# Performance work log

Measured on AMD Instinct MI355X. Metric: run time of the kernel, lower is better.

Reference implementation:

```python
import jax, jax.numpy as jnp
from jax import lax
import numpy as np

B, T, NCLS, D = 64, 2048, 20, 2048
LCS_LEN, FSD_LEN = 64, 32
LAMB1, LAMB2, LAMB3 = 1.0, 5e-5, 8e-5
LAMB_LCS, LAMB_FSD = 0.01, 0.01
FEAT_MARGIN = 50.0
THRES = 0.5
GAMMA = 0.1


def cos_sim(a, b):
    a = a / jnp.linalg.norm(a, axis=1, keepdims=True)
    b = b / jnp.linalg.norm(b, axis=1, keepdims=True)
    return a @ b.T


def dp_fsd(c0, c1):
    # soft-LCS/DTW-style recurrence with maxGamma (soft max) over 3 neighbors
    h = c0.shape[-1] // 2
    m = cos_sim(c0[:, :h], c1[:, :h])  # [L, L]
    g = cos_sim(c0[:, h:], c1[:, h:])  # [L, L]
    L = m.shape[0]

    def row_step(prev_row, mg):
        m_row, g_row = mg
        diag = prev_row[:-1]  # C[i-1, j-1]
        up = prev_row[1:]     # C[i-1, j]

        def col_step(left, xs):  # left = C[i, j-1]
            d, u, mij, gij = xs
            neigh = jnp.stack([d, gij + u, gij + left])
            val = mij + GAMMA * jax.nn.logsumexp(neigh / GAMMA)
            return val, val

        _, row_vals = lax.scan(col_step, jnp.zeros((), m.dtype), (diag, up, m_row, g_row))
        new_row = jnp.concatenate([jnp.zeros((1,), m.dtype), row_vals])
        return new_row, None

    final_row, _ = lax.scan(row_step, jnp.zeros(L + 1, m.dtype), (m, g))
    return final_row[-1]


def dp_lcs(c0, c1):
    s = cos_sim(c0, c1)  # [L, L]
    L = s.shape[0]

    def row_step(prev_row, s_row):
        diag = prev_row[:-1]
        up = prev_row[1:]

        def col_step(left, xs):
            d, u, sij = xs
            val = jnp.where(sij > THRES, d + sij, jnp.maximum(u, left))
            return val, val

        _, row_vals = lax.scan(col_step, jnp.zeros((), s.dtype), (diag, up, s_row))
        return jnp.concatenate([jnp.zeros((1,), s.dtype), row_vals]), None

    final_row, _ = lax.scan(row_step, jnp.zeros(L + 1, s.dtype), s)
    return final_row[-1]


def cls_criterion(p, lab):
    return -jnp.mean(jnp.sum(jnp.log(p + 1e-10) * lab, axis=1))


def forward_once(ai_cls, ac_cls, ab_cls, vlab, att, ai_feat, ac_feat, ab_feat, ai_cas):
    bs = ai_cls.shape[0]
    ones = jnp.ones((bs, 1), ai_cls.dtype)
    zeros = jnp.zeros((bs, 1), ai_cls.dtype)
    inst_lab = jnp.concatenate([vlab, zeros], axis=1)
    cont_lab = jnp.concatenate([vlab, ones], axis=1)
    back_lab = jnp.concatenate([jnp.zeros_like(vlab), ones], axis=1)
    inst_lab = inst_lab / jnp.sum(inst_lab, axis=1, keepdims=True)
    cont_lab = cont_lab / jnp.sum(cont_lab, axis=1, keepdims=True)
    back_lab = back_lab / jnp.sum(back_lab, axis=1, keepdims=True)

    inst_loss = cls_criterion(ai_cls, inst_lab)
    cont_loss = cls_criterion(ac_cls, cont_lab)
    back_loss = cls_criterion(ab_cls, back_lab)

    guide_loss = jnp.mean(jnp.sum(jnp.abs(1.0 - ai_cas[:, :, -1] - lax.stop_gradient(att[:, :, 0])), axis=1))

    n_inst = jnp.linalg.norm(ai_feat, axis=1)
    n_cont = jnp.linalg.norm(ac_feat, axis=1)
    n_back = jnp.linalg.norm(ab_feat, axis=1)
    f1 = jnp.maximum(FEAT_MARGIN - n_inst + n_cont, 0.0)
    f2 = jnp.maximum(FEAT_MARGIN - n_cont + n_back, 0.0)
    f3 = n_back
    feat_loss = jnp.mean((f1 + f2 + f3) ** 2)

    sparse_loss = jnp.mean(jnp.sum(att[:, :, :2], axis=1))

    cls_loss = inst_loss + cont_loss + back_loss  # THUMOS14 weights 1/1/1
    return cls_loss + LAMB1 * guide_loss + LAMB2 * feat_loss + LAMB3 * sparse_loss


def _pair_loss(vals, pair_label):
    bs = vals.shape[0]
    pos = jnp.sum(vals * pair_label)
    neg = jnp.sum(vals * (1.0 - pair_label))
    pos_num = jnp.sum(pair_label)
    neg_num = bs - pos_num
    return neg / (neg_num + 1e-10) - pos / (pos_num + 1e-10)


def ftcl_forward(act_inst_cls_0, act_cont_cls_0, act_back_cls_0, vid_label_0, temp_att_0,
                 act_inst_feat_0, act_cont_feat_0, act_back_feat_0, act_inst_cas_0,
                 lcs_candi_0, fsd_act_candi_0, fsd_bak_candi_0,
                 act_inst_cls_1, act_cont_cls_1, act_back_cls_1, vid_label_1, temp_att_1,
                 act_inst_feat_1, act_cont_feat_1, act_back_feat_1, act_inst_cas_1,
                 lcs_candi_1, fsd_act_candi_1, fsd_bak_candi_1):
    loss_0 = forward_once(act_inst_cls_0, act_cont_cls_0, act_back_cls_0, vid_label_0, temp_att_0,
                          act_inst_feat_0, act_cont_feat_0, act_back_feat_0, act_inst_cas_0)
    loss_1 = forward_once(act_inst_cls_1, act_cont_cls_1, act_back_cls_1, vid_label_1, temp_att_1,
                          act_inst_feat_1, act_cont_feat_1, act_back_feat_1, act_inst_cas_1)
    acm_loss = (loss_0 + loss_1) / 2.0

    pair_label = (jnp.sum(vid_label_0 * vid_label_1, axis=1) > 0).astype(jnp.float32)  # [B]

    lcs = jax.vmap(dp_lcs)(lcs_candi_0, lcs_candi_1)  # [B]
    lcs_loss = _pair_loss(lcs, pair_label)

    # pair==1 -> act_1, pair==0 -> bak_1 (matches the per-sample branch in torch)
    fsd_c1 = jnp.where(pair_label[:, None, None] > 0, fsd_act_candi_1, fsd_bak_candi_1)
    fsd = jax.vmap(dp_fsd)(fsd_act_candi_0, fsd_c1)  # [B]
    fsd_loss = _pair_loss(fsd, pair_label)

    return acm_loss + LAMB_LCS * lcs_loss + LAMB_FSD * fsd_loss


def setup_inputs() -> dict:
    key = jax.random.key(0)
    ks = iter(jax.random.split(key, 32))
    rand = lambda s: jax.random.uniform(next(ks), s, jnp.float32)
    randn = lambda s: jax.random.normal(next(ks), s, jnp.float32)
    inp = {}
    for sfx in ('0', '1'):
        inp[f'act_inst_cls_{sfx}'] = rand((B, NCLS + 1))
        inp[f'act_cont_cls_{sfx}'] = rand((B, NCLS + 1))
        inp[f'act_back_cls_{sfx}'] = rand((B, NCLS + 1))
        inp[f'vid_label_{sfx}'] = jnp.ones((B, NCLS), jnp.float32)
        inp[f'temp_att_{sfx}'] = rand((B, T, 3))
        inp[f'act_inst_feat_{sfx}'] = randn((B, D))
        inp[f'act_cont_feat_{sfx}'] = randn((B, D))
        inp[f'act_back_feat_{sfx}'] = randn((B, D))
        inp[f'act_inst_cas_{sfx}'] = rand((B, T, NCLS + 1))
        inp[f'lcs_candi_{sfx}'] = randn((B, LCS_LEN, D))
        inp[f'fsd_act_candi_{sfx}'] = randn((B, FSD_LEN, D))
        inp[f'fsd_bak_candi_{sfx}'] = randn((B, FSD_LEN, D))
    return inp


def reference(act_inst_cls_0, act_cont_cls_0, act_back_cls_0, vid_label_0, temp_att_0,
              act_inst_feat_0, act_cont_feat_0, act_back_feat_0, act_inst_cas_0,
              lcs_candi_0, fsd_act_candi_0, fsd_bak_candi_0,
              act_inst_cls_1, act_cont_cls_1, act_back_cls_1, vid_label_1, temp_att_1,
              act_inst_feat_1, act_cont_feat_1, act_back_feat_1, act_inst_cas_1,
              lcs_candi_1, fsd_act_candi_1, fsd_bak_candi_1):
    return ftcl_forward(act_inst_cls_0, act_cont_cls_0, act_back_cls_0, vid_label_0, temp_att_0,
                        act_inst_feat_0, act_cont_feat_0, act_back_feat_0, act_inst_cas_0,
                        lcs_candi_0, fsd_act_candi_0, fsd_bak_candi_0,
                        act_inst_cls_1, act_cont_cls_1, act_back_cls_1, vid_label_1, temp_att_1,
                        act_inst_feat_1, act_cont_feat_1, act_back_feat_1, act_inst_cas_1,
                        lcs_candi_1, fsd_act_candi_1, fsd_bak_candi_1)
```

## Files before the change

### kernel.cpp

```cpp
#include <hip/hip_runtime.h>
#include <math.h>

#define Bn 64
#define Tn 2048
#define NCLS 20
#define Dn 2048
#define LCSL 64
#define FSDL 32

#define KS_L 8
#define KS_F 4

#define WS_ACC 0
#define WS_PAIR 4
#define WS_LCS 68
#define WS_FSD 132
#define WS_NORM 196
#define WS_LSQ 580
#define WS_FSQ 66116
#define WS_SPART 98884
#define WS_MG 2196036

__global__ __launch_bounds__(256) void fused_small_kernel(
    const float* __restrict__ cas0, const float* __restrict__ att0,
    const float* __restrict__ cas1, const float* __restrict__ att1,
    const float* __restrict__ f0, const float* __restrict__ f1,
    const float* __restrict__ f2, const float* __restrict__ f3,
    const float* __restrict__ f4, const float* __restrict__ f5,
    const float* __restrict__ vid0, const float* __restrict__ vid1,
    float* __restrict__ ws) {
    const int gb = blockIdx.x;
    const int t = threadIdx.x;
    if (gb < 512) {
        const int N = Bn * Tn;
        float g0 = 0.f, s0 = 0.f, g1 = 0.f, s1 = 0.f;
        for (int n = gb * 256 + t; n < 2 * N; n += 512 * 256) {
            int sfx = (n >= N);
            int m = sfx ? (n - N) : n;
            const float* cas = sfx ? cas1 : cas0;
            const float* att = sfx ? att1 : att0;
            float a0 = att[m * 3 + 0];
            float a1 = att[m * 3 + 1];
            float g = fabsf(1.0f - cas[m * (NCLS + 1) + NCLS] - a0);
            float s = a0 + a1;
            if (sfx) { g1 += g; s1 += s; } else { g0 += g; s0 += s; }
        }
        __shared__ float red[256];
        float vals[4] = {g0, s0, g1, s1};
        for (int v = 0; v < 4; ++v) {
            red[t] = vals[v];
            __syncthreads();
            for (int o = 128; o; o >>= 1) {
                if (t < o) red[t] += red[t + o];
                __syncthreads();
            }
            if (t == 0) atomicAdd(&ws[WS_ACC + v], red[0]);
            __syncthreads();
        }
    } else if (gb < 608) {
        int R = (gb - 512) * 4 + (t >> 6);
        int lane = t & 63;
        const float* arr[6] = {f0, f1, f2, f3, f4, f5};
        const float* p = arr[R >> 6] + (size_t)(R & 63) * Dn;
        float s = 0.f;
        #pragma unroll
        for (int q = 0; q < 8; ++q) {
            float4 v = *(const float4*)(p + q * 256 + lane * 4);
            s += v.x * v.x + v.y * v.y + v.z * v.z + v.w * v.w;
        }
        for (int off = 32; off; off >>= 1) s += __shfl_down(s, off);
        if (lane == 0) ws[WS_NORM + R] = sqrtf(s);
    } else {
        if (t < Bn) {
            float s = 0.f;
            for (int c = 0; c < NCLS; ++c) s += vid0[t * NCLS + c] * vid1[t * NCLS + c];
            ws[WS_PAIR + t] = (s > 0.f) ? 1.f : 0.f;
        }
    }
}

__global__ __launch_bounds__(256) void gemm_kernel(const float* __restrict__ cand0,
                                                   const float* __restrict__ cand1,
                                                   const float* __restrict__ act0,
                                                   const float* __restrict__ act1,
                                                   const float* __restrict__ bak1,
                                                   float* __restrict__ ws) {
    __shared__ float tA[64 * 66];
    __shared__ float tB[64 * 66];
    const int t = threadIdx.x;

    if (blockIdx.x < 512) {
        const int b = blockIdx.x >> 3;
        const int ks = blockIdx.x & 7;
        const float* c0 = cand0 + (size_t)b * LCSL * Dn + ks * 256;
        const float* c1 = cand1 + (size_t)b * LCSL * Dn + ks * 256;

        const int ti = t >> 4, tj = t & 15;
        const int i0 = ti * 4, j0 = tj * 4;
        float acc[4][4] = {};
        float sqa[4] = {}, sqb[4] = {};

        for (int kc = 0; kc < 256; kc += 64) {
            #pragma unroll
            for (int l = 0; l < 4; ++l) {
                int idx4 = l * 256 + t;
                int row = idx4 >> 4;
                int kq = (idx4 & 15) * 4;
                float4 av = *(const float4*)(c0 + (size_t)row * Dn + kc + kq);
                float4 bv = *(const float4*)(c1 + (size_t)row * Dn + kc + kq);
                tA[(kq + 0) * 66 + row] = av.x;
                tA[(kq + 1) * 66 + row] = av.y;
                tA[(kq + 2) * 66 + row] = av.z;
                tA[(kq + 3) * 66 + row] = av.w;
                tB[(kq + 0) * 66 + row] = bv.x;
                tB[(kq + 1) * 66 + row] = bv.y;
                tB[(kq + 2) * 66 + row] = bv.z;
                tB[(kq + 3) * 66 + row] = bv.w;
                sqa[l] += av.x * av.x + av.y * av.y + av.z * av.z + av.w * av.w;
                sqb[l] += bv.x * bv.x + bv.y * bv.y + bv.z * bv.z + bv.w * bv.w;
            }
            __syncthreads();
            #pragma unroll 8
            for (int k = 0; k < 64; ++k) {
                float2 a0v = *(const float2*)&tA[k * 66 + i0];
                float2 a1v = *(const float2*)&tA[k * 66 + i0 + 2];
                float2 b0v = *(const float2*)&tB[k * 66 + j0];
                float2 b1v = *(const float2*)&tB[k * 66 + j0 + 2];
                float a[4] = {a0v.x, a0v.y, a1v.x, a1v.y};
                float bb[4] = {b0v.x, b0v.y, b1v.x, b1v.y};
                #pragma unroll
                for (int r = 0; r < 4; ++r)
                    #pragma unroll
                    for (int c = 0; c < 4; ++c)
                        acc[r][c] = fmaf(a[r], bb[c], acc[r][c]);
            }
            __syncthreads();
        }
        float* dst = ws + WS_SPART + (size_t)(ks * Bn + b) * 4096;
        #pragma unroll
        for (int r = 0; r < 4; ++r) {
            float4 v = {acc[r][0], acc[r][1], acc[r][2], acc[r][3]};
            *(float4*)(dst + (i0 + r) * 64 + j0) = v;
        }
        #pragma unroll
        for (int l = 0; l < 4; ++l) {
            float sa = sqa[l], sb = sqb[l];
            for (int m = 1; m < 16; m <<= 1) {
                sa += __shfl_xor(sa, m);
                sb += __shfl_xor(sb, m);
            }
            if ((t & 15) == 0) {
                int row = l * 16 + (t >> 4);
                ws[WS_LSQ + ks * 8192 + b * 128 + row] = sa;
                ws[WS_LSQ + ks * 8192 + b * 128 + 64 + row] = sb;
            }
        }
    } else {
        const int q = blockIdx.x - 512;
        const int b = q >> 3;
        const int half = (q >> 2) & 1;
        const int ks = q & 3;
        const float* pairp = ws + WS_PAIR;
        const int sel = (pairp[b] > 0.f) ? 1 : 2;
        const float* c0 = act0 + (size_t)b * FSDL * Dn + half * 1024 + ks * 256;
        const float* c1 = ((sel == 1) ? act1 : bak1) + (size_t)b * FSDL * Dn + half * 1024 + ks * 256;

        const int ti = t >> 4, tj = t & 15;
        const int i0 = ti * 2, j0 = tj * 2;
        float acc[2][2] = {};
        float sqa[2] = {}, sqb[2] = {};

        for (int kc = 0; kc < 256; kc += 64) {
            #pragma unroll
            for (int l = 0; l < 2; ++l) {
                int idx4 = l * 256 + t;
                int row = idx4 >> 4;
                int kq = (idx4 & 15) * 4;
                float4 av = *(const float4*)(c0 + (size_t)row * Dn + kc + kq);
                float4 bv = *(const float4*)(c1 + (size_t)row * Dn + kc + kq);
                tA[(kq + 0) * 34 + row] = av.x;
                tA[(kq + 1) * 34 + row] = av.y;
                tA[(kq + 2) * 34 + row] = av.z;
                tA[(kq + 3) * 34 + row] = av.w;
                tB[(kq + 0) * 34 + row] = bv.x;
                tB[(kq + 1) * 34 + row] = bv.y;
                tB[(kq + 2) * 34 + row] = bv.z;
                tB[(kq + 3) * 34 + row] = bv.w;
                sqa[l] += av.x * av.x + av.y * av.y + av.z * av.z + av.w * av.w;
                sqb[l] += bv.x * bv.x + bv.y * bv.y + bv.z * bv.z + bv.w * bv.w;
            }
            __syncthreads();
            #pragma unroll 8
            for (int k = 0; k < 64; ++k) {
                float2 a = *(const float2*)&tA[k * 34 + i0];
                float2 bb = *(const float2*)&tB[k * 34 + j0];
                acc[0][0] = fmaf(a.x, bb.x, acc[0][0]);
                acc[0][1] = fmaf(a.x, bb.y, acc[0][1]);
                acc[1][0] = fmaf(a.y, bb.x, acc[1][0]);
                acc[1][1] = fmaf(a.y, bb.y, acc[1][1]);
            }
            __syncthreads();
        }
        float* dst = ws + WS_MG + (size_t)ks * 131072 + b * 2048 + half * 1024;
        #pragma unroll
        for (int r = 0; r < 2; ++r) {
            float2 v = {acc[r][0], acc[r][1]};
            *(float2*)(dst + (i0 + r) * 32 + j0) = v;
        }
        #pragma unroll
        for (int l = 0; l < 2; ++l) {
            float sa = sqa[l], sb = sqb[l];
            for (int m = 1; m < 16; m <<= 1) {
                sa += __shfl_xor(sa, m);
                sb += __shfl_xor(sb, m);
            }
            if ((t & 15) == 0) {
                int row = l * 16 + (t >> 4);
                ws[WS_FSQ + ks * 8192 + b * 128 + half * 64 + row] = sa;
                ws[WS_FSQ + ks * 8192 + b * 128 + half * 64 + 32 + row] = sb;
            }
        }
    }
}

__global__ __launch_bounds__(64) void dp_kernel(float* __restrict__ ws) {
    const int t = threadIdx.x;
    if (blockIdx.x < 64) {
        const int b = blockIdx.x;
        __shared__ float S[64 * 66];
        __shared__ float i0s[64], i1s[64];
        {
            float s0 = 0.f, s1 = 0.f;
            #pragma unroll
            for (int ks = 0; ks < KS_L; ++ks) {
                s0 += ws[WS_LSQ + ks * 8192 + b * 128 + t];
                s1 += ws[WS_LSQ + ks * 8192 + b * 128 + 64 + t];
            }
            i0s[t] = 1.0f / sqrtf(s0);
            i1s[t] = 1.0f / sqrtf(s1);
        }
        __syncthreads();
        const float* sp = ws + WS_SPART + b * 4096;
        for (int qd = 0; qd < 16; ++qd) {
            int idx4 = t + 64 * qd;
            int i = idx4 >> 4;
            int j = (idx4 & 15) * 4;
            float4 v = {0.f, 0.f, 0.f, 0.f};
            #pragma unroll
            for (int ks = 0; ks < KS_L; ++ks) {
                float4 p = *(const float4*)(sp + (size_t)ks * 262144 + idx4 * 4);
                v.x += p.x; v.y += p.y; v.z += p.z; v.w += p.w;
            }
            float ri = i0s[i];
            S[i * 66 + j + 0] = v.x * ri * i1s[j + 0];
            S[i * 66 + j + 1] = v.y * ri * i1s[j + 1];
            S[i * 66 + j + 2] = v.z * ri * i1s[j + 2];
            S[i * 66 + j + 3] = v.w * ri * i1s[j + 3];
        }
        __syncthreads();
        float prev = 0.f, prevprev = 0.f;
        float sval_next = S[t * 66 + 0];
        for (int d = 2; d <= 128; ++d) {
            float s = sval_next;
            int jn = d - t - 1;
            if (jn >= 0 && jn < 64) sval_next = S[t * 66 + jn];
            float up = __shfl_up(prev, 1);
            float dg = __shfl_up(prevprev, 1);
            if (t == 0) { up = 0.f; dg = 0.f; }
            int j = d - t - 1;
            float left = prev;
            float val = (s > 0.5f) ? (dg + s) : fmaxf(up, left);
            float cur = (j >= 1 && j <= 64) ? val : 0.f;
            prevprev = prev;
            prev = cur;
        }
        if (t == 63) ws[WS_LCS + b] = prev;
    } else {
        const int b = blockIdx.x - 64;
        __shared__ float M[32 * 34], G[32 * 34];
        __shared__ float inv[128];
        {
            #pragma unroll
            for (int e2 = 0; e2 < 2; ++e2) {
                int e = t + e2 * 64;
                float s = 0.f;
                #pragma unroll
                for (int ks = 0; ks < KS_F; ++ks)
                    s += ws[WS_FSQ + ks * 8192 + b * 128 + e];
                inv[e] = 1.0f / sqrtf(s);
            }
        }
        __syncthreads();
        const float* mg = ws + WS_MG + b * 2048;
        for (int qd = 0; qd < 4; ++qd) {
            int idx4 = t + 64 * qd;
            int i = idx4 >> 3;
            int j = (idx4 & 7) * 4;
            float4 vM = {0.f, 0.f, 0.f, 0.f}, vG = {0.f, 0.f, 0.f, 0.f};
            #pragma unroll
            for (int ks = 0; ks < KS_F; ++ks) {
                float4 pM = *(const float4*)(mg + (size_t)ks * 131072 + idx4 * 4);
                float4 pG = *(const float4*)(mg + (size_t)ks * 131072 + 1024 + idx4 * 4);
                vM.x += pM.x; vM.y += pM.y; vM.z += pM.z; vM.w += pM.w;
                vG.x += pG.x; vG.y += pG.y; vG.z += pG.z; vG.w += pG.w;
            }
            float riM = inv[i], riG = inv[64 + i];
            M[i * 34 + j + 0] = vM.x * riM * inv[32 + j + 0];
            M[i * 34 + j + 1] = vM.y * riM * inv[32 + j + 1];
            M[i * 34 + j + 2] = vM.z * riM * inv[32 + j + 2];
            M[i * 34 + j + 3] = vM.w * riM * inv[32 + j + 3];
            G[i * 34 + j + 0] = vG.x * riG * inv[96 + j + 0];
            G[i * 34 + j + 1] = vG.y * riG * inv[96 + j + 1];
            G[i * 34 + j + 2] = vG.z * riG * inv[96 + j + 2];
            G[i * 34 + j + 3] = vG.w * riG * inv[96 + j + 3];
        }
        __syncthreads();
        if (t < 32) {
            float prev = 0.f, prevprev = 0.f;
            float m_next = M[t * 34 + 0], g_next = G[t * 34 + 0];
            for (int d = 2; d <= 64; ++d) {
                float m = m_next, g = g_next;
                int jn = d - t - 1;
                if (jn >= 0 && jn < 32) { m_next = M[t * 34 + jn]; g_next = G[t * 34 + jn]; }
                float up = __shfl_up(prev, 1);
                float dg = __shfl_up(prevprev, 1);
                if (t == 0) { up = 0.f; dg = 0.f; }
                int j = d - t - 1;
                float left = prev;
                float x0 = dg * 10.0f;
                float x1 = (g + up) * 10.0f;
                float x2 = (g + left) * 10.0f;
                float mx = fmaxf(x0, fmaxf(x1, x2));
                float lse = mx + __logf(__expf(x0 - mx) + __expf(x1 - mx) + __expf(x2 - mx));
                float val = m + 0.1f * lse;
                float cur = (j >= 1 && j <= 32) ? val : 0.f;
                prevprev = prev;
                prev = cur;
            }
            if (t == 31) ws[WS_FSD + b] = prev;
        }
    }
}

__device__ float block_reduce(float v, float* red, int t) {
    red[t] = v;
    __syncthreads();
    for (int o = 128; o; o >>= 1) {
        if (t < o) red[t] += red[t + o];
        __syncthreads();
    }
    float r = red[0];
    __syncthreads();
    return r;
}

__global__ __launch_bounds__(256) void final_kernel(
    const float* __restrict__ ai0, const float* __restrict__ ac0,
    const float* __restrict__ ab0, const float* __restrict__ vid0,
    const float* __restrict__ ai1, const float* __restrict__ ac1,
    const float* __restrict__ ab1, const float* __restrict__ vid1,
    const float* __restrict__ ws, float* __restrict__ out) {
    __shared__ float rs0[Bn], rs1[Bn];
    __shared__ float red[256];
    int t = threadIdx.x;
    if (t < Bn) {
        float s0 = 0.f, s1 = 0.f;
        for (int c = 0; c < NCLS; ++c) { s0 += vid0[t * NCLS + c]; s1 += vid1[t * NCLS + c]; }
        rs0[t] = s0;
        rs1[t] = s1;
    }
    __syncthreads();

    float inst0 = 0.f, cont0 = 0.f, back0 = 0.f;
    float inst1 = 0.f, cont1 = 0.f, back1 = 0.f;
    for (int idx = t; idx < Bn * (NCLS + 1); idx += 256) {
        int b = idx / (NCLS + 1), c = idx % (NCLS + 1);
        float v0 = (c < NCLS) ? vid0[b * NCLS + c] : 0.f;
        float v1 = (c < NCLS) ? vid1[b * NCLS + c] : 0.f;
        float wI0 = (c < NCLS) ? (v0 / rs0[b]) : 0.f;
        float wC0 = ((c < NCLS) ? v0 : 1.f) / (rs0[b] + 1.f);
        float wI1 = (c < NCLS) ? (v1 / rs1[b]) : 0.f;
        float wC1 = ((c < NCLS) ? v1 : 1.f) / (rs1[b] + 1.f);
        inst0 += logf(ai0[idx] + 1e-10f) * wI0;
        cont0 += logf(ac0[idx] + 1e-10f) * wC0;
        inst1 += logf(ai1[idx] + 1e-10f) * wI1;
        cont1 += logf(ac1[idx] + 1e-10f) * wC1;
        if (c == NCLS) {
            back0 += logf(ab0[idx] + 1e-10f);
            back1 += logf(ab1[idx] + 1e-10f);
        }
    }
    float sInst0 = block_reduce(inst0, red, t);
    float sCont0 = block_reduce(cont0, red, t);
    float sBack0 = block_reduce(back0, red, t);
    float sInst1 = block_reduce(inst1, red, t);
    float sCont1 = block_reduce(cont1, red, t);
    float sBack1 = block_reduce(back1, red, t);

    float fv0 = 0.f, fv1 = 0.f;
    if (t < Bn) {
        const float* nm = ws + WS_NORM;
        {
            float ni = nm[0 * Bn + t], nc = nm[1 * Bn + t], nb = nm[2 * Bn + t];
            float f1 = fmaxf(50.0f - ni + nc, 0.f);
            float f2 = fmaxf(50.0f - nc + nb, 0.f);
            float f = f1 + f2 + nb;
            fv0 = f * f;
        }
        {
            float ni = nm[3 * Bn + t], nc = nm[4 * Bn + t], nb = nm[5 * Bn + t];
            float f1 = fmaxf(50.0f - ni + nc, 0.f);
            float f2 = fmaxf(50.0f - nc + nb, 0.f);
            float f = f1 + f2 + nb;
            fv1 = f * f;
        }
    }
    float sFeat0 = block_reduce(fv0, red, t) / (float)Bn;
    float sFeat1 = block_reduce(fv1, red, t) / (float)Bn;

    float posL = 0.f, negL = 0.f, posF = 0.f, negF = 0.f, pln = 0.f;
    if (t < Bn) {
        float pl = ws[WS_PAIR + t];
        float lv = ws[WS_LCS + t];
        float fv = ws[WS_FSD + t];
        posL = lv * pl; negL = lv * (1.f - pl);
        posF = fv * pl; negF = fv * (1.f - pl);
        pln = pl;
    }
    float sPosL = block_reduce(posL, red, t);
    float sNegL = block_reduce(negL, red, t);
    float sPosF = block_reduce(posF, red, t);
    float sNegF = block_reduce(negF, red, t);
    float sPln = block_reduce(pln, red, t);

    if (t == 0) {
        float cls0 = -(sInst0 + sCont0 + sBack0) / (float)Bn;
        float cls1 = -(sInst1 + sCont1 + sBack1) / (float)Bn;
        float guide0 = ws[WS_ACC + 0] / (float)Bn;
        float sparse0 = ws[WS_ACC + 1] / (float)(Bn * 2);
        float guide1 = ws[WS_ACC + 2] / (float)Bn;
        float sparse1 = ws[WS_ACC + 3] / (float)(Bn * 2);
        float loss0 = cls0 + 1.0f * guide0 + 5e-05f * sFeat0 + 8e-05f * sparse0;
        float loss1 = cls1 + 1.0f * guide1 + 5e-05f * sFeat1 + 8e-05f * sparse1;
        float acm = 0.5f * (loss0 + loss1);
        float posn = sPln;
        float negn = (float)Bn - posn;
        float lcs_loss = sNegL / (negn + 1e-10f) - sPosL / (posn + 1e-10f);
        float fsd_loss = sNegF / (negn + 1e-10f) - sPosF / (posn + 1e-10f);
        out[0] = acm + 0.01f * lcs_loss + 0.01f * fsd_loss;
    }
}

extern "C" void kernel_launch(void* const* d_in, const int* in_sizes, int n_in,
                              void* d_out, int out_size, void* d_ws, size_t ws_size,
                              hipStream_t stream) {
    (void)in_sizes; (void)n_in; (void)out_size; (void)ws_size;
    const float* ai0  = (const float*)d_in[0];
    const float* ac0  = (const float*)d_in[1];
    const float* ab0  = (const float*)d_in[2];
    const float* vid0 = (const float*)d_in[3];
    const float* att0 = (const float*)d_in[4];
    const float* fi0  = (const float*)d_in[5];
    const float* fc0  = (const float*)d_in[6];
    const float* fb0  = (const float*)d_in[7];
    const float* cas0 = (const float*)d_in[8];
    const float* lcs0 = (const float*)d_in[9];
    const float* fsdA0 = (const float*)d_in[10];
    const float* ai1  = (const float*)d_in[12];
    const float* ac1  = (const float*)d_in[13];
    const float* ab1  = (const float*)d_in[14];
    const float* vid1 = (const float*)d_in[15];
    const float* att1 = (const float*)d_in[16];
    const float* fi1  = (const float*)d_in[17];
    const float* fc1  = (const float*)d_in[18];
    const float* fb1  = (const float*)d_in[19];
    const float* cas1 = (const float*)d_in[20];
    const float* lcs1 = (const float*)d_in[21];
    const float* fsdA1 = (const float*)d_in[22];
    const float* fsdB1 = (const float*)d_in[23];

    float* ws = (float*)d_ws;

    hipMemsetAsync(d_ws, 0, 4 * sizeof(float), stream);
    fused_small_kernel<<<609, 256, 0, stream>>>(cas0, att0, cas1, att1,
                                                fi0, fc0, fb0, fi1, fc1, fb1,
                                                vid0, vid1, ws);
    gemm_kernel<<<1024, 256, 0, stream>>>(lcs0, lcs1, fsdA0, fsdA1, fsdB1, ws);
    dp_kernel<<<128, 64, 0, stream>>>(ws);
    final_kernel<<<1, 256, 0, stream>>>(ai0, ac0, ab0, vid0, ai1, ac1, ab1, vid1, ws,
                                        (float*)d_out);
}
```

Before: 271.7 us.

## Fuse small reductions and GEMMs into one kernel, swizzle shared tiles

Merges the small reduction kernel and the GEMM kernel into a single launch. Each GEMM block now recomputes the pair label itself, and the guide/sparse sums are written as per-block partials instead of via atomics, so the memset is dropped. The shared-memory tiles get XOR swizzling, smaller K chunks for the LCS part and float4 reads, and the workspace layout is reordered so each batch's partials sit together. The DP kernel moves to 256 threads to parallelise the normalisation step, and the final kernel reduces the partial sums. The aim is to cut launch count, atomics and bank conflicts, at the cost of more register and shared-memory pressure in one kernel.

```diff
diff --git a/kernel.cpp b/kernel.cpp
--- a/kernel.cpp
+++ b/kernel.cpp
@@ -8,33 +8,178 @@
 #define LCSL 64
 #define FSDL 32
 
-#define KS_L 8
-#define KS_F 4
-
-#define WS_ACC 0
-#define WS_PAIR 4
-#define WS_LCS 68
-#define WS_FSD 132
-#define WS_NORM 196
-#define WS_LSQ 580
-#define WS_FSQ 66116
-#define WS_SPART 98884
-#define WS_MG 2196036
-
-__global__ __launch_bounds__(256) void fused_small_kernel(
+#define WS_LCS 0
+#define WS_FSD 64
+#define WS_NORM 128
+#define WS_GS 512
+#define WS_LSQ 1024
+#define WS_FSQ 66560
+#define WS_SPART 99328
+#define WS_MG 2196480
+
+__global__ __launch_bounds__(256) void mega_kernel(
+    const float* __restrict__ lcs0, const float* __restrict__ lcs1,
+    const float* __restrict__ fA0, const float* __restrict__ fA1,
+    const float* __restrict__ fB1,
+    const float* __restrict__ vid0, const float* __restrict__ vid1,
     const float* __restrict__ cas0, const float* __restrict__ att0,
     const float* __restrict__ cas1, const float* __restrict__ att1,
     const float* __restrict__ f0, const float* __restrict__ f1,
     const float* __restrict__ f2, const float* __restrict__ f3,
     const float* __restrict__ f4, const float* __restrict__ f5,
-    const float* __restrict__ vid0, const float* __restrict__ vid1,
     float* __restrict__ ws) {
-    const int gb = blockIdx.x;
+    __shared__ float tA[2176];
+    __shared__ float tB[2176];
     const int t = threadIdx.x;
-    if (gb < 512) {
+    const int bid = blockIdx.x;
+
+    if (bid < 512) {
+        const int b = bid >> 3, ks = bid & 7;
+        const float* c0 = lcs0 + (size_t)b * LCSL * Dn + ks * 256;
+        const float* c1 = lcs1 + (size_t)b * LCSL * Dn + ks * 256;
+        const int ti = t >> 4, tj = t & 15;
+        const int i0 = ti * 4, j0 = tj * 4;
+        float acc[4][4] = {};
+        float sqa0 = 0.f, sqa1 = 0.f, sqb0 = 0.f, sqb1 = 0.f;
+
+        for (int kc = 0; kc < 256; kc += 32) {
+            __syncthreads();
+            #pragma unroll
+            for (int l = 0; l < 2; ++l) {
+                int idx4 = l * 256 + t;
+                int row = idx4 >> 3;
+                int kq = (idx4 & 7) * 4;
+                float4 av = *(const float4*)(c0 + (size_t)row * Dn + kc + kq);
+                float4 bv = *(const float4*)(c1 + (size_t)row * Dn + kc + kq);
+                int rowx = row ^ kq;
+                tA[(kq + 0) * 68 + rowx] = av.x;
+                tA[(kq + 1) * 68 + rowx] = av.y;
+                tA[(kq + 2) * 68 + rowx] = av.z;
+                tA[(kq + 3) * 68 + rowx] = av.w;
+                tB[(kq + 0) * 68 + rowx] = bv.x;
+                tB[(kq + 1) * 68 + rowx] = bv.y;
+                tB[(kq + 2) * 68 + rowx] = bv.z;
+                tB[(kq + 3) * 68 + rowx] = bv.w;
+                float sa = av.x * av.x + av.y * av.y + av.z * av.z + av.w * av.w;
+                float sb = bv.x * bv.x + bv.y * bv.y + bv.z * bv.z + bv.w * bv.w;
+                if (l == 0) { sqa0 += sa; sqb0 += sb; }
+                else        { sqa1 += sa; sqb1 += sb; }
+            }
+            __syncthreads();
+            #pragma unroll 8
+            for (int k = 0; k < 32; ++k) {
+                int sk = k & 28;
+                float4 a4 = *(const float4*)&tA[k * 68 + (i0 ^ sk)];
+                float4 b4 = *(const float4*)&tB[k * 68 + (j0 ^ sk)];
+                float a[4] = {a4.x, a4.y, a4.z, a4.w};
+                float bb[4] = {b4.x, b4.y, b4.z, b4.w};
+                #pragma unroll
+                for (int r = 0; r < 4; ++r)
+                    #pragma unroll
+                    for (int c = 0; c < 4; ++c)
+                        acc[r][c] = fmaf(a[r], bb[c], acc[r][c]);
+            }
+        }
+        float* dst = ws + WS_SPART + (size_t)(b * 8 + ks) * 4096;
+        #pragma unroll
+        for (int r = 0; r < 4; ++r) {
+            float4 v = {acc[r][0], acc[r][1], acc[r][2], acc[r][3]};
+            *(float4*)(dst + (i0 + r) * 64 + j0) = v;
+        }
+        #pragma unroll
+        for (int m = 1; m < 8; m <<= 1) {
+            sqa0 += __shfl_xor(sqa0, m);
+            sqa1 += __shfl_xor(sqa1, m);
+            sqb0 += __shfl_xor(sqb0, m);
+            sqb1 += __shfl_xor(sqb1, m);
+        }
+        if ((t & 7) == 0) {
+            int r0 = t >> 3;
+            float* q = ws + WS_LSQ + (size_t)(b * 8 + ks) * 128;
+            q[r0] = sqa0;
+            q[r0 + 32] = sqa1;
+            q[64 + r0] = sqb0;
+            q[96 + r0] = sqb1;
+        }
+    } else if (bid < 1024) {
+        const int q = bid - 512;
+        const int b = q >> 3, half = (q >> 2) & 1, ks = q & 3;
+        float ps = 0.f;
+        for (int c = 0; c < NCLS; ++c) ps += vid0[b * NCLS + c] * vid1[b * NCLS + c];
+        const float* base1 = (ps > 0.f) ? fA1 : fB1;
+        const float* c0 = fA0 + (size_t)b * FSDL * Dn + half * 1024 + ks * 256;
+        const float* c1 = base1 + (size_t)b * FSDL * Dn + half * 1024 + ks * 256;
+        const int ti = t >> 4, tj = t & 15;
+        const int i0 = ti * 2, j0 = tj * 2;
+        float acc[2][2] = {};
+        float sqa0 = 0.f, sqa1 = 0.f, sqb0 = 0.f, sqb1 = 0.f;
+
+        for (int kc = 0; kc < 256; kc += 64) {
+            __syncthreads();
+            #pragma unroll
+            for (int l = 0; l < 2; ++l) {
+                int idx4 = l * 256 + t;
+                int row = idx4 >> 4;
+                int kq = (idx4 & 15) * 4;
+                float4 av = *(const float4*)(c0 + (size_t)row * Dn + kc + kq);
+                float4 bv = *(const float4*)(c1 + (size_t)row * Dn + kc + kq);
+                {
+                    int r0x = row ^ ((kq + 0) & 30);
+                    int r1x = row ^ ((kq + 1) & 30);
+                    int r2x = row ^ ((kq + 2) & 30);
+                    int r3x = row ^ ((kq + 3) & 30);
+                    tA[(kq + 0) * 34 + r0x] = av.x;
+                    tA[(kq + 1) * 34 + r1x] = av.y;
+                    tA[(kq + 2) * 34 + r2x] = av.z;
+                    tA[(kq + 3) * 34 + r3x] = av.w;
+                    tB[(kq + 0) * 34 + r0x] = bv.x;
+                    tB[(kq + 1) * 34 + r1x] = bv.y;
+                    tB[(kq + 2) * 34 + r2x] = bv.z;
+                    tB[(kq + 3) * 34 + r3x] = bv.w;
+                }
+                float sa = av.x * av.x + av.y * av.y + av.z * av.z + av.w * av.w;
+                float sb = bv.x * bv.x + bv.y * bv.y + bv.z * bv.z + bv.w * bv.w;
+                if (l == 0) { sqa0 += sa; sqb0 += sb; }
+                else        { sqa1 += sa; sqb1 += sb; }
+            }
+            __syncthreads();
+            #pragma unroll 8
+            for (int k = 0; k < 64; ++k) {
+                int sk = k & 30;
+                float2 a2 = *(const float2*)&tA[k * 34 + (i0 ^ sk)];
+                float2 b2 = *(const float2*)&tB[k * 34 + (j0 ^ sk)];
+                acc[0][0] = fmaf(a2.x, b2.x, acc[0][0]);
+                acc[0][1] = fmaf(a2.x, b2.y, acc[0][1]);
+                acc[1][0] = fmaf(a2.y, b2.x, acc[1][0]);
+                acc[1][1] = fmaf(a2.y, b2.y, acc[1][1]);
+            }
+        }
+        float* dst = ws + WS_MG + (size_t)((b * 2 + half) * 4 + ks) * 1024;
+        #pragma unroll
+        for (int r = 0; r < 2; ++r) {
+            float2 v = {acc[r][0], acc[r][1]};
+            *(float2*)(dst + (i0 + r) * 32 + j0) = v;
+        }
+        #pragma unroll
+        for (int m = 1; m < 16; m <<= 1) {
+            sqa0 += __shfl_xor(sqa0, m);
+            sqa1 += __shfl_xor(sqa1, m);
+            sqb0 += __shfl_xor(sqb0, m);
+            sqb1 += __shfl_xor(sqb1, m);
+        }
+        if ((t & 15) == 0) {
+            int r0 = t >> 4;
+            float* qq = ws + WS_FSQ + (size_t)((b * 2 + half) * 4 + ks) * 64;
+            qq[r0] = sqa0;
+            qq[r0 + 16] = sqa1;
+            qq[32 + r0] = sqb0;
+            qq[48 + r0] = sqb1;
+        }
+    } else if (bid < 1152) {
+        const int gb = bid - 1024;
         const int N = Bn * Tn;
         float g0 = 0.f, s0 = 0.f, g1 = 0.f, s1 = 0.f;
-        for (int n = gb * 256 + t; n < 2 * N; n += 512 * 256) {
+        for (int n = gb * 256 + t; n < 2 * N; n += 128 * 256) {
             int sfx = (n >= N);
             int m = sfx ? (n - N) : n;
             const float* cas = sfx ? cas1 : cas0;
@@ -45,283 +190,127 @@
             float s = a0 + a1;
             if (sfx) { g1 += g; s1 += s; } else { g0 += g; s0 += s; }
         }
-        __shared__ float red[256];
         float vals[4] = {g0, s0, g1, s1};
-        for (int v = 0; v < 4; ++v) {
-            red[t] = vals[v];
+        #pragma unroll
+        for (int v = 0; v < 4; ++v) tA[v * 256 + t] = vals[v];
+        __syncthreads();
+        for (int o = 128; o; o >>= 1) {
+            if (t < o) {
+                #pragma unroll
+                for (int v = 0; v < 4; ++v) tA[v * 256 + t] += tA[v * 256 + t + o];
+            }
             __syncthreads();
-            for (int o = 128; o; o >>= 1) {
-                if (t < o) red[t] += red[t + o];
-                __syncthreads();
-            }
-            if (t == 0) atomicAdd(&ws[WS_ACC + v], red[0]);
-            __syncthreads();
-        }
-    } else if (gb < 608) {
-        int R = (gb - 512) * 4 + (t >> 6);
+        }
+        if (t < 4) ws[WS_GS + gb * 4 + t] = tA[t * 256];
+    } else {
+        int R = (bid - 1152) * 4 + (t >> 6);
         int lane = t & 63;
         const float* arr[6] = {f0, f1, f2, f3, f4, f5};
         const float* p = arr[R >> 6] + (size_t)(R & 63) * Dn;
         float s = 0.f;
         #pragma unroll
-        for (int q = 0; q < 8; ++q) {
-            float4 v = *(const float4*)(p + q * 256 + lane * 4);
+        for (int qd = 0; qd < 8; ++qd) {
+            float4 v = *(const float4*)(p + qd * 256 + lane * 4);
             s += v.x * v.x + v.y * v.y + v.z * v.z + v.w * v.w;
         }
         for (int off = 32; off; off >>= 1) s += __shfl_down(s, off);
         if (lane == 0) ws[WS_NORM + R] = sqrtf(s);
-    } else {
-        if (t < Bn) {
-            float s = 0.f;
-            for (int c = 0; c < NCLS; ++c) s += vid0[t * NCLS + c] * vid1[t * NCLS + c];
-            ws[WS_PAIR + t] = (s > 0.f) ? 1.f : 0.f;
-        }
     }
 }
 
-__global__ __launch_bounds__(256) void gemm_kernel(const float* __restrict__ cand0,
-                                                   const float* __restrict__ cand1,
-                                                   const float* __restrict__ act0,
-                                                   const float* __restrict__ act1,
-                                                   const float* __restrict__ bak1,
-                                                   float* __restrict__ ws) {
-    __shared__ float tA[64 * 66];
-    __shared__ float tB[64 * 66];
-    const int t = threadIdx.x;
-
-    if (blockIdx.x < 512) {
-        const int b = blockIdx.x >> 3;
-        const int ks = blockIdx.x & 7;
-        const float* c0 = cand0 + (size_t)b * LCSL * Dn + ks * 256;
-        const float* c1 = cand1 + (size_t)b * LCSL * Dn + ks * 256;
-
-        const int ti = t >> 4, tj = t & 15;
-        const int i0 = ti * 4, j0 = tj * 4;
-        float acc[4][4] = {};
-        float sqa[4] = {}, sqb[4] = {};
-
-        for (int kc = 0; kc < 256; kc += 64) {
-            #pragma unroll
-            for (int l = 0; l < 4; ++l) {
-                int idx4 = l * 256 + t;
-                int row = idx4 >> 4;
-                int kq = (idx4 & 15) * 4;
-                float4 av = *(const float4*)(c0 + (size_t)row * Dn + kc + kq);
-                float4 bv = *(const float4*)(c1 + (size_t)row * Dn + kc + kq);
-                tA[(kq + 0) * 66 + row] = av.x;
-                tA[(kq + 1) * 66 + row] = av.y;
-                tA[(kq + 2) * 66 + row] = av.z;
-                tA[(kq + 3) * 66 + row] = av.w;
-                tB[(kq + 0) * 66 + row] = bv.x;
-                tB[(kq + 1) * 66 + row] = bv.y;
-                tB[(kq + 2) * 66 + row] = bv.z;
-                tB[(kq + 3) * 66 + row] = bv.w;
-                sqa[l] += av.x * av.x + av.y * av.y + av.z * av.z + av.w * av.w;
-                sqb[l] += bv.x * bv.x + bv.y * bv.y + bv.z * bv.z + bv.w * bv.w;
-            }
-            __syncthreads();
-            #pragma unroll 8
-            for (int k = 0; k < 64; ++k) {
-                float2 a0v = *(const float2*)&tA[k * 66 + i0];
-                float2 a1v = *(const float2*)&tA[k * 66 + i0 + 2];
-                float2 b0v = *(const float2*)&tB[k * 66 + j0];
-                float2 b1v = *(const float2*)&tB[k * 66 + j0 + 2];
-                float a[4] = {a0v.x, a0v.y, a1v.x, a1v.y};
-                float bb[4] = {b0v.x, b0v.y, b1v.x, b1v.y};
-                #pragma unroll
-                for (int r = 0; r < 4; ++r)
-                    #pragma unroll
-                    for (int c = 0; c < 4; ++c)
-                        acc[r][c] = fmaf(a[r], bb[c], acc[r][c]);
-            }
-            __syncthreads();
-        }
-        float* dst = ws + WS_SPART + (size_t)(ks * Bn + b) * 4096;
-        #pragma unroll
-        for (int r = 0; r < 4; ++r) {
-            float4 v = {acc[r][0], acc[r][1], acc[r][2], acc[r][3]};
-            *(float4*)(dst + (i0 + r) * 64 + j0) = v;
-        }
-        #pragma unroll
-        for (int l = 0; l < 4; ++l) {
-            float sa = sqa[l], sb = sqb[l];
-            for (int m = 1; m < 16; m <<= 1) {
-                sa += __shfl_xor(sa, m);
-                sb += __shfl_xor(sb, m);
-            }
-            if ((t & 15) == 0) {
-                int row = l * 16 + (t >> 4);
-                ws[WS_LSQ + ks * 8192 + b * 128 + row] = sa;
-                ws[WS_LSQ + ks * 8192 + b * 128 + 64 + row] = sb;
-            }
-        }
-    } else {
-        const int q = blockIdx.x - 512;
-        const int b = q >> 3;
-        const int half = (q >> 2) & 1;
-        const int ks = q & 3;
-        const float* pairp = ws + WS_PAIR;
-        const int sel = (pairp[b] > 0.f) ? 1 : 2;
-        const float* c0 = act0 + (size_t)b * FSDL * Dn + half * 1024 + ks * 256;
-        const float* c1 = ((sel == 1) ? act1 : bak1) + (size_t)b * FSDL * Dn + half * 1024 + ks * 256;
-
-        const int ti = t >> 4, tj = t & 15;
-        const int i0 = ti * 2, j0 = tj * 2;
-        float acc[2][2] = {};
-        float sqa[2] = {}, sqb[2] = {};
-
-        for (int kc = 0; kc < 256; kc += 64) {
-            #pragma unroll
-            for (int l = 0; l < 2; ++l) {
-                int idx4 = l * 256 + t;
-                int row = idx4 >> 4;
-                int kq = (idx4 & 15) * 4;
-                float4 av = *(const float4*)(c0 + (size_t)row * Dn + kc + kq);
-                float4 bv = *(const float4*)(c1 + (size_t)row * Dn + kc + kq);
-                tA[(kq + 0) * 34 + row] = av.x;
-                tA[(kq + 1) * 34 + row] = av.y;
-                tA[(kq + 2) * 34 + row] = av.z;
-                tA[(kq + 3) * 34 + row] = av.w;
-                tB[(kq + 0) * 34 + row] = bv.x;
-                tB[(kq + 1) * 34 + row] = bv.y;
-                tB[(kq + 2) * 34 + row] = bv.z;
-                tB[(kq + 3) * 34 + row] = bv.w;
-                sqa[l] += av.x * av.x + av.y * av.y + av.z * av.z + av.w * av.w;
-                sqb[l] += bv.x * bv.x + bv.y * bv.y + bv.z * bv.z + bv.w * bv.w;
-            }
-            __syncthreads();
-            #pragma unroll 8
-            for (int k = 0; k < 64; ++k) {
-                float2 a = *(const float2*)&tA[k * 34 + i0];
-                float2 bb = *(const float2*)&tB[k * 34 + j0];
-                acc[0][0] = fmaf(a.x, bb.x, acc[0][0]);
-                acc[0][1] = fmaf(a.x, bb.y, acc[0][1]);
-                acc[1][0] = fmaf(a.y, bb.x, acc[1][0]);
-                acc[1][1] = fmaf(a.y, bb.y, acc[1][1]);
-            }
-            __syncthreads();
-        }
-        float* dst = ws + WS_MG + (size_t)ks * 131072 + b * 2048 + half * 1024;
-        #pragma unroll
-        for (int r = 0; r < 2; ++r) {
-            float2 v = {acc[r][0], acc[r][1]};
-            *(float2*)(dst + (i0 + r) * 32 + j0) = v;
-        }
-        #pragma unroll
-        for (int l = 0; l < 2; ++l) {
-            float sa = sqa[l], sb = sqb[l];
-            for (int m = 1; m < 16; m <<= 1) {
-                sa += __shfl_xor(sa, m);
-                sb += __shfl_xor(sb, m);
-            }
-            if ((t & 15) == 0) {
-                int row = l * 16 + (t >> 4);
-                ws[WS_FSQ + ks * 8192 + b * 128 + half * 64 + row] = sa;
-                ws[WS_FSQ + ks * 8192 + b * 128 + half * 64 + 32 + row] = sb;
-            }
-        }
-    }
-}
-
-__global__ __launch_bounds__(64) void dp_kernel(float* __restrict__ ws) {
+__global__ __launch_bounds__(256) void dp_kernel(float* __restrict__ ws) {
     const int t = threadIdx.x;
     if (blockIdx.x < 64) {
         const int b = blockIdx.x;
-        __shared__ float S[64 * 66];
-        __shared__ float i0s[64], i1s[64];
-        {
-            float s0 = 0.f, s1 = 0.f;
-            #pragma unroll
-            for (int ks = 0; ks < KS_L; ++ks) {
-                s0 += ws[WS_LSQ + ks * 8192 + b * 128 + t];
-                s1 += ws[WS_LSQ + ks * 8192 + b * 128 + 64 + t];
-            }
-            i0s[t] = 1.0f / sqrtf(s0);
-            i1s[t] = 1.0f / sqrtf(s1);
-        }
-        __syncthreads();
-        const float* sp = ws + WS_SPART + b * 4096;
-        for (int qd = 0; qd < 16; ++qd) {
-            int idx4 = t + 64 * qd;
-            int i = idx4 >> 4;
-            int j = (idx4 & 15) * 4;
+        __shared__ float S[64 * 68];
+        __shared__ float inv[128];
+        if (t < 128) {
+            float s = 0.f;
+            #pragma unroll
+            for (int ks = 0; ks < 8; ++ks)
+                s += ws[WS_LSQ + (size_t)(b * 8 + ks) * 128 + t];
+            inv[t] = 1.0f / sqrtf(s);
+        }
+        __syncthreads();
+        const float* sp = ws + WS_SPART + (size_t)b * 32768;
+        #pragma unroll
+        for (int qd = 0; qd < 4; ++qd) {
+            int idx4 = qd * 256 + t;
+            int i = idx4 >> 4, j = (idx4 & 15) * 4;
             float4 v = {0.f, 0.f, 0.f, 0.f};
             #pragma unroll
-            for (int ks = 0; ks < KS_L; ++ks) {
-                float4 p = *(const float4*)(sp + (size_t)ks * 262144 + idx4 * 4);
+            for (int ks = 0; ks < 8; ++ks) {
+                float4 p = *(const float4*)(sp + (size_t)ks * 4096 + idx4 * 4);
                 v.x += p.x; v.y += p.y; v.z += p.z; v.w += p.w;
             }
-            float ri = i0s[i];
-            S[i * 66 + j + 0] = v.x * ri * i1s[j + 0];
-            S[i * 66 + j + 1] = v.y * ri * i1s[j + 1];
-            S[i * 66 + j + 2] = v.z * ri * i1s[j + 2];
-            S[i * 66 + j + 3] = v.w * ri * i1s[j + 3];
-        }
-        __syncthreads();
-        float prev = 0.f, prevprev = 0.f;
-        float sval_next = S[t * 66 + 0];
-        for (int d = 2; d <= 128; ++d) {
-            float s = sval_next;
-            int jn = d - t - 1;
-            if (jn >= 0 && jn < 64) sval_next = S[t * 66 + jn];
-            float up = __shfl_up(prev, 1);
-            float dg = __shfl_up(prevprev, 1);
-            if (t == 0) { up = 0.f; dg = 0.f; }
-            int j = d - t - 1;
-            float left = prev;
-            float val = (s > 0.5f) ? (dg + s) : fmaxf(up, left);
-            float cur = (j >= 1 && j <= 64) ? val : 0.f;
-            prevprev = prev;
-            prev = cur;
-        }
-        if (t == 63) ws[WS_LCS + b] = prev;
+            float ri = inv[i];
+            S[i * 68 + j + 0] = v.x * ri * inv[64 + j + 0];
+            S[i * 68 + j + 1] = v.y * ri * inv[64 + j + 1];
+            S[i * 68 + j + 2] = v.z * ri * inv[64 + j + 2];
+            S[i * 68 + j + 3] = v.w * ri * inv[64 + j + 3];
+        }
+        __syncthreads();
+        if (t < 64) {
+            float prev = 0.f, prevprev = 0.f;
+            float sval_next = S[t * 68 + 0];
+            for (int d = 2; d <= 128; ++d) {
+                float s = sval_next;
+                int jn = d - t - 1;
+                if (jn >= 0 && jn < 64) sval_next = S[t * 68 + jn];
+                float up = __shfl_up(prev, 1);
+                float dg = __shfl_up(prevprev, 1);
+                if (t == 0) { up = 0.f; dg = 0.f; }
+                int j = d - t - 1;
+                float left = prev;
+                float val = (s > 0.5f) ? (dg + s) : fmaxf(up, left);
+                float cur = (j >= 1 && j <= 64) ? val : 0.f;
+                prevprev = prev;
+                prev = cur;
+            }
+            if (t == 63) ws[WS_LCS + b] = prev;
+        }
     } else {
         const int b = blockIdx.x - 64;
-        __shared__ float M[32 * 34], G[32 * 34];
+        __shared__ float M[32 * 36], G[32 * 36];
         __shared__ float inv[128];
+        if (t < 128) {
+            int half = t >> 6, sub = t & 63;
+            float s = 0.f;
+            #pragma unroll
+            for (int ks = 0; ks < 4; ++ks)
+                s += ws[WS_FSQ + (size_t)((b * 2 + half) * 4 + ks) * 64 + sub];
+            inv[t] = 1.0f / sqrtf(s);
+        }
+        __syncthreads();
         {
-            #pragma unroll
-            for (int e2 = 0; e2 < 2; ++e2) {
-                int e = t + e2 * 64;
-                float s = 0.f;
-                #pragma unroll
-                for (int ks = 0; ks < KS_F; ++ks)
-                    s += ws[WS_FSQ + ks * 8192 + b * 128 + e];
-                inv[e] = 1.0f / sqrtf(s);
-            }
-        }
-        __syncthreads();
-        const float* mg = ws + WS_MG + b * 2048;
-        for (int qd = 0; qd < 4; ++qd) {
-            int idx4 = t + 64 * qd;
-            int i = idx4 >> 3;
-            int j = (idx4 & 7) * 4;
+            int idx4 = t;
+            int i = idx4 >> 3, j = (idx4 & 7) * 4;
             float4 vM = {0.f, 0.f, 0.f, 0.f}, vG = {0.f, 0.f, 0.f, 0.f};
             #pragma unroll
-            for (int ks = 0; ks < KS_F; ++ks) {
-                float4 pM = *(const float4*)(mg + (size_t)ks * 131072 + idx4 * 4);
-                float4 pG = *(const float4*)(mg + (size_t)ks * 131072 + 1024 + idx4 * 4);
+            for (int ks = 0; ks < 4; ++ks) {
+                float4 pM = *(const float4*)(ws + WS_MG + (size_t)((b * 2 + 0) * 4 + ks) * 1024 + idx4 * 4);
+                float4 pG = *(const float4*)(ws + WS_MG + (size_t)((b * 2 + 1) * 4 + ks) * 1024 + idx4 * 4);
                 vM.x += pM.x; vM.y += pM.y; vM.z += pM.z; vM.w += pM.w;
                 vG.x += pG.x; vG.y += pG.y; vG.z += pG.z; vG.w += pG.w;
             }
             float riM = inv[i], riG = inv[64 + i];
-            M[i * 34 + j + 0] = vM.x * riM * inv[32 + j + 0];
-            M[i * 34 + j + 1] = vM.y * riM * inv[32 + j + 1];
-            M[i * 34 + j + 2] = vM.z * riM * inv[32 + j + 2];
-            M[i * 34 + j + 3] = vM.w * riM * inv[32 + j + 3];
-            G[i * 34 + j + 0] = vG.x * riG * inv[96 + j + 0];
-            G[i * 34 + j + 1] = vG.y * riG * inv[96 + j + 1];
-            G[i * 34 + j + 2] = vG.z * riG * inv[96 + j + 2];
-            G[i * 34 + j + 3] = vG.w * riG * inv[96 + j + 3];
+            M[i * 36 + j + 0] = vM.x * riM * inv[32 + j + 0];
+            M[i * 36 + j + 1] = vM.y * riM * inv[32 + j + 1];
+            M[i * 36 + j + 2] = vM.z * riM * inv[32 + j + 2];
+            M[i * 36 + j + 3] = vM.w * riM * inv[32 + j + 3];
+            G[i * 36 + j + 0] = vG.x * riG * inv[96 + j + 0];
+            G[i * 36 + j + 1] = vG.y * riG * inv[96 + j + 1];
+            G[i * 36 + j + 2] = vG.z * riG * inv[96 + j + 2];
+            G[i * 36 + j + 3] = vG.w * riG * inv[96 + j + 3];
         }
         __syncthreads();
         if (t < 32) {
             float prev = 0.f, prevprev = 0.f;
-            float m_next = M[t * 34 + 0], g_next = G[t * 34 + 0];
+            float m_next = M[t * 36 + 0], g_next = G[t * 36 + 0];
             for (int d = 2; d <= 64; ++d) {
                 float m = m_next, g = g_next;
                 int jn = d - t - 1;
-                if (jn >= 0 && jn < 32) { m_next = M[t * 34 + jn]; g_next = G[t * 34 + jn]; }
+                if (jn >= 0 && jn < 32) { m_next = M[t * 36 + jn]; g_next = G[t * 36 + jn]; }
                 float up = __shfl_up(prev, 1);
                 float dg = __shfl_up(prevprev, 1);
                 if (t == 0) { up = 0.f; dg = 0.f; }
@@ -360,14 +349,18 @@
     const float* __restrict__ ai1, const float* __restrict__ ac1,
     const float* __restrict__ ab1, const float* __restrict__ vid1,
     const float* __restrict__ ws, float* __restrict__ out) {
-    __shared__ float rs0[Bn], rs1[Bn];
+    __shared__ float rs0[Bn], rs1[Bn], plsh[Bn];
     __shared__ float red[256];
     int t = threadIdx.x;
     if (t < Bn) {
-        float s0 = 0.f, s1 = 0.f;
-        for (int c = 0; c < NCLS; ++c) { s0 += vid0[t * NCLS + c]; s1 += vid1[t * NCLS + c]; }
+        float s0 = 0.f, s1 = 0.f, pp = 0.f;
+        for (int c = 0; c < NCLS; ++c) {
+            float a = vid0[t * NCLS + c], bl = vid1[t * NCLS + c];
+            s0 += a; s1 += bl; pp += a * bl;
+        }
         rs0[t] = s0;
         rs1[t] = s1;
+        plsh[t] = (pp > 0.f) ? 1.f : 0.f;
     }
     __syncthreads();
 
@@ -397,6 +390,18 @@
     float sCont1 = block_reduce(cont1, red, t);
     float sBack1 = block_reduce(back1, red, t);
 
+    float g0 = 0.f, s0v = 0.f, g1 = 0.f, s1v = 0.f;
+    for (int i = t; i < 128; i += 256) {
+        g0  += ws[WS_GS + i * 4 + 0];
+        s0v += ws[WS_GS + i * 4 + 1];
+        g1  += ws[WS_GS + i * 4 + 2];
+        s1v += ws[WS_GS + i * 4 + 3];
+    }
+    float sG0 = block_reduce(g0, red, t);
+    float sS0 = block_reduce(s0v, red, t);
+    float sG1 = block_reduce(g1, red, t);
+    float sS1 = block_reduce(s1v, red, t);
+
     float fv0 = 0.f, fv1 = 0.f;
     if (t < Bn) {
         const float* nm = ws + WS_NORM;
@@ -420,7 +425,7 @@
 
     float posL = 0.f, negL = 0.f, posF = 0.f, negF = 0.f, pln = 0.f;
     if (t < Bn) {
-        float pl = ws[WS_PAIR + t];
+        float pl = plsh[t];
         float lv = ws[WS_LCS + t];
         float fv = ws[WS_FSD + t];
         posL = lv * pl; negL = lv * (1.f - pl);
@@ -436,10 +441,10 @@
     if (t == 0) {
         float cls0 = -(sInst0 + sCont0 + sBack0) / (float)Bn;
         float cls1 = -(sInst1 + sCont1 + sBack1) / (float)Bn;
-        float guide0 = ws[WS_ACC + 0] / (float)Bn;
-        float sparse0 = ws[WS_ACC + 1] / (float)(Bn * 2);
-        float guide1 = ws[WS_ACC + 2] / (float)Bn;
-        float sparse1 = ws[WS_ACC + 3] / (float)(Bn * 2);
+        float guide0 = sG0 / (float)Bn;
+        float sparse0 = sS0 / (float)(Bn * 2);
+        float guide1 = sG1 / (float)Bn;
+        float sparse1 = sS1 / (float)(Bn * 2);
         float loss0 = cls0 + 1.0f * guide0 + 5e-05f * sFeat0 + 8e-05f * sparse0;
         float loss1 = cls1 + 1.0f * guide1 + 5e-05f * sFeat1 + 8e-05f * sparse1;
         float acm = 0.5f * (loss0 + loss1);
@@ -481,12 +486,10 @@
 
     float* ws = (float*)d_ws;
 
-    hipMemsetAsync(d_ws, 0, 4 * sizeof(float), stream);
-    fused_small_kernel<<<609, 256, 0, stream>>>(cas0, att0, cas1, att1,
-                                                fi0, fc0, fb0, fi1, fc1, fb1,
-                                                vid0, vid1, ws);
-    gemm_kernel<<<1024, 256, 0, stream>>>(lcs0, lcs1, fsdA0, fsdA1, fsdB1, ws);
-    dp_kernel<<<128, 64, 0, stream>>>(ws);
+    mega_kernel<<<1248, 256, 0, stream>>>(lcs0, lcs1, fsdA0, fsdA1, fsdB1,
+                                          vid0, vid1, cas0, att0, cas1, att1,
+                                          fi0, fc0, fb0, fi1, fc1, fb1, ws);
+    dp_kernel<<<128, 256, 0, stream>>>(ws);
     final_kernel<<<1, 256, 0, stream>>>(ai0, ac0, ab0, vid0, ai1, ac1, ab1, vid1, ws,
                                         (float*)d_out);
 }
```

Measured after the change: 244.3 us. 1.11x faster.
